# Kernel optimization log

Hardware: AMD Instinct MI355X
Metric: run time of the kernel (lower is better)

## Reference

```python
import jax, jax.numpy as jnp
import numpy as np

EMB_DIM = 128
NUM_CLS = 128
H = W = 512
K = 131072


def setup_inputs() -> dict:
    key = jax.random.key(0)
    k1, k2, k3, k4 = jax.random.split(key, 4)
    gc_features = jax.random.normal(k1, (1, EMB_DIM, H, W), dtype=jnp.float32)
    cls_id_map = jax.random.randint(k2, (1, K), 0, H * W, dtype=jnp.int64)
    # nn.Linear(emb_dim, num_cls) params, kaiming-uniform-ish scale
    lim = 1.0 / np.sqrt(EMB_DIM)
    W_cls = jax.random.uniform(k3, (NUM_CLS, EMB_DIM), dtype=jnp.float32, minval=-lim, maxval=lim)
    b_cls = jax.random.uniform(k4, (NUM_CLS,), dtype=jnp.float32, minval=-lim, maxval=lim)
    return {"gc_features": gc_features, "cls_id_map": cls_id_map, "W_cls": W_cls, "b_cls": b_cls}


def reference(gc_features, cls_id_map, W_cls, b_cls):
    B, C, h, w = gc_features.shape
    # _tranpose_and_gather_feat: [B,C,H,W] -> [B,HW,C], gather rows by inds
    feat = gc_features.reshape(B, C, h * w).transpose(0, 2, 1)      # [B, HW, C]
    feat = jnp.take_along_axis(feat, cls_id_map[:, :, None], axis=1)  # [B, K, C]
    feat = feat[0]                                                   # squeeze(0) -> [K, C]
    pred = feat @ W_cls.T + b_cls                                    # [K, num_cls]
    return jax.nn.softmax(pred, axis=1)
```

## Files before the change

kernel.cpp:

```cpp
#include <hip/hip_runtime.h>
#include <hip/hip_bf16.h>
#include <hip/hip_fp16.h>

#define HW      262144
#define NCH     128
#define NCLS    128
#define KROWS   131072
#define BM      64
#define OLP     144

typedef short  bf16x8 __attribute__((ext_vector_type(8)));
typedef float  f32x4  __attribute__((ext_vector_type(4)));

__device__ inline ushort f2bf(float f) {
    union { float f; unsigned u; } v; v.f = f;
    unsigned u = v.u;
    unsigned r = (u + 0x7FFFu + ((u >> 16) & 1u)) >> 16;
    return (ushort)r;
}

__global__ __launch_bounds__(256) void wconv(const float* __restrict__ Wc,
                                             ushort* __restrict__ Wf) {
    int e    = blockIdx.x * 256 + threadIdx.x;
    int j    = e & 7;
    int slot = e >> 3;
    int lane = slot & 63;
    int kk   = (slot >> 6) & 3;
    int nt   = slot >> 8;
    int n = (nt << 4) + (lane & 15);
    int k = (kk << 5) + ((lane >> 4) << 3) + j;
    Wf[e] = f2bf(Wc[n * NCH + k]);
}

__global__ __launch_bounds__(256) void gemm_probs(const float* __restrict__ gc,
                                                  const ushort* __restrict__ Wf,
                                                  const float* __restrict__ bias,
                                                  ushort* __restrict__ pred) {
    __shared__ ushort Wl[NCLS * NCH];
    __shared__ ushort AO[BM * OLP];

    const int t    = threadIdx.x;
    const int lane = t & 63;
    const int wv   = t >> 6;
    const int l15  = lane & 15;

    #pragma unroll
    for (int i = 0; i < 8; ++i) {
        const ushort* g = Wf + (i << 11) + (t << 3);
        ushort*       l = Wl + (i << 11) + (t << 3);
        __builtin_amdgcn_global_load_lds(
            (const __attribute__((address_space(1))) unsigned*)g,
            (__attribute__((address_space(3))) unsigned*)l, 16, 0, 0);
    }

    float bcol[8];
    #pragma unroll
    for (int nt = 0; nt < 8; ++nt) bcol[nt] = bias[(nt << 4) + l15];

    for (int tile = 0; tile < 2; ++tile) {
        const int m0 = (blockIdx.x * 2 + tile) * BM;

        __syncthreads();

        #pragma unroll
        for (int i = 0; i < 4; ++i) {
            int q  = (i << 8) + t;
            int cp = q >> 4;
            int mq = q & 15;
            int c0 = cp << 1;
            int m  = mq << 2;
            float4 v0 = *(const float4*)&gc[(size_t)c0 * HW + m0 + m];
            float4 v1 = *(const float4*)&gc[(size_t)(c0 + 1) * HW + m0 + m];
            int kk = c0 >> 5;
            int hi = ((c0 >> 3) & 3) << 4;
            int j  = c0 & 7;
            const float* a0 = (const float*)&v0;
            const float* a1 = (const float*)&v1;
            #pragma unroll
            for (int d = 0; d < 4; ++d) {
                int row   = m + d;
                int lslot = (row & 15) + hi;
                int mt    = row >> 4;
                int addr  = ((((mt << 2) + kk) << 6) + lslot) << 3;
                __hip_bfloat162 pk = __float22bfloat162_rn(make_float2(a0[d], a1[d]));
                *(ushort2*)&AO[addr + j] = *(ushort2*)&pk;
            }
        }
        __syncthreads();

        f32x4 acc[8];
        #pragma unroll
        for (int i = 0; i < 8; ++i) acc[i] = (f32x4){0.f, 0.f, 0.f, 0.f};

        #pragma unroll
        for (int kk = 0; kk < 4; ++kk) {
            bf16x8 a = *(const bf16x8*)&AO[((((wv << 2) + kk) << 6) + lane) << 3];
            #pragma unroll
            for (int nt = 0; nt < 8; ++nt) {
                bf16x8 b = *(const bf16x8*)&Wl[((((nt << 2) + kk) << 6) + lane) << 3];
                acc[nt] = __builtin_amdgcn_mfma_f32_16x16x32_bf16(a, b, acc[nt], 0, 0, 0);
            }
        }

        float pr[8][4];
        #pragma unroll
        for (int rr = 0; rr < 4; ++rr) {
            float ex[8], s = 0.f;
            #pragma unroll
            for (int nt = 0; nt < 8; ++nt) {
                ex[nt] = __expf(acc[nt][rr] + bcol[nt]);
                s += ex[nt];
            }
            s += __shfl_xor(s, 1, 64);
            s += __shfl_xor(s, 2, 64);
            s += __shfl_xor(s, 4, 64);
            s += __shfl_xor(s, 8, 64);
            float inv = 1.0f / s;
            #pragma unroll
            for (int nt = 0; nt < 8; ++nt) pr[nt][rr] = ex[nt] * inv;
        }

        __syncthreads();

        const int rowb = (wv << 4) + ((lane >> 4) << 2);
        #pragma unroll
        for (int nt = 0; nt < 8; ++nt)
            #pragma unroll
            for (int rr = 0; rr < 4; ++rr)
                AO[(rowb + rr) * OLP + (nt << 4) + l15] =
                    __half_as_ushort(__float2half_rn(pr[nt][rr]));
        __syncthreads();

        #pragma unroll
        for (int i = 0; i < 4; ++i) {
            int q   = (i << 8) + t;
            int row = q >> 4;
            int ch  = q & 15;
            int4 v = *(const int4*)&AO[row * OLP + (ch << 3)];
            *(int4*)&pred[(size_t)(m0 + row) * NCLS + (ch << 3)] = v;
        }
    }
}

__global__ __launch_bounds__(256) void gather_rows(const ushort* __restrict__ pred,
                                                   const int* __restrict__ idx,
                                                   float* __restrict__ out) {
    const int t    = threadIdx.x;
    const int lane = t & 63;
    const int wv   = t >> 6;
    const int kbase = (blockIdx.x << 4) + (wv << 2);

    int p[4];
    #pragma unroll
    for (int r = 0; r < 4; ++r) p[r] = idx[kbase + r];

    #pragma unroll
    for (int r = 0; r < 4; ++r) {
        __half2 h = *(const __half2*)&pred[(size_t)p[r] * NCLS + (lane << 1)];
        float2 f = __half22float2(h);
        *(float2*)&out[(size_t)(kbase + r) * NCLS + (lane << 1)] = f;
    }
}

extern "C" void kernel_launch(void* const* d_in, const int* in_sizes, int n_in,
                              void* d_out, int out_size, void* d_ws, size_t ws_size,
                              hipStream_t stream) {
    const float* gc   = (const float*)d_in[0];
    const int*   idx  = (const int*)d_in[1];
    const float* Wc   = (const float*)d_in[2];
    const float* bias = (const float*)d_in[3];
    float*  out  = (float*)d_out;
    ushort* pred = (ushort*)d_ws;

    ushort* Wf = (ushort*)d_out;

    wconv<<<dim3(64), dim3(256), 0, stream>>>(Wc, Wf);
    gemm_probs<<<dim3(HW / (2 * BM)), dim3(256), 0, stream>>>(gc, Wf, bias, pred);
    gather_rows<<<dim3(KROWS / 16), dim3(256), 0, stream>>>(pred, idx, out);
}
```

Before: 243.4 us.

## Replace pred buffer and gather with CSR inverse index and fused scatter

Builds a CSR inverse map from pixel to output rows using a histogram, a three-stage prefix scan and an atomic fill. The GEMM+softmax kernel then scatters each probability row straight into every output row that references it, so the fp16 pred intermediate is never written to or reread from global memory. This trades that round trip for six extra small kernel launches, atomics, and scattered, divergent per-row writes.

```diff
diff --git a/kernel.cpp b/kernel.cpp
--- a/kernel.cpp
+++ b/kernel.cpp
@@ -17,6 +17,79 @@
     unsigned u = v.u;
     unsigned r = (u + 0x7FFFu + ((u >> 16) & 1u)) >> 16;
     return (ushort)r;
+}
+
+
+__global__ __launch_bounds__(256) void csr_zero(int4* __restrict__ cnt4) {
+    cnt4[blockIdx.x * 256 + threadIdx.x] = make_int4(0, 0, 0, 0);
+}
+
+__global__ __launch_bounds__(256) void csr_hist(const int* __restrict__ idx,
+                                                int* __restrict__ cnt) {
+    int k = blockIdx.x * 256 + threadIdx.x;
+    atomicAdd(&cnt[idx[k]], 1);
+}
+
+__global__ __launch_bounds__(256) void scan_a(const int* __restrict__ cnt,
+                                              int* __restrict__ off,
+                                              int* __restrict__ bsum) {
+    __shared__ int s[256];
+    const int t = threadIdx.x;
+    const int base = blockIdx.x * 256;
+    int v = cnt[base + t];
+    s[t] = v;
+    __syncthreads();
+    #pragma unroll
+    for (int o = 1; o < 256; o <<= 1) {
+        int add = (t >= o) ? s[t - o] : 0;
+        __syncthreads();
+        s[t] += add;
+        __syncthreads();
+    }
+    off[base + t] = s[t] - v;
+    if (t == 255) bsum[blockIdx.x] = s[255];
+}
+
+__global__ __launch_bounds__(256) void scan_b(int* __restrict__ bsum) {
+    __shared__ int s[256];
+    const int t = threadIdx.x;
+    int4 v = ((int4*)bsum)[t];
+    int sum4 = v.x + v.y + v.z + v.w;
+    s[t] = sum4;
+    __syncthreads();
+    #pragma unroll
+    for (int o = 1; o < 256; o <<= 1) {
+        int add = (t >= o) ? s[t - o] : 0;
+        __syncthreads();
+        s[t] += add;
+        __syncthreads();
+    }
+    int base = s[t] - sum4;
+    int4 o;
+    o.x = base;
+    o.y = base + v.x;
+    o.z = base + v.x + v.y;
+    o.w = base + v.x + v.y + v.z;
+    ((int4*)bsum)[t] = o;
+}
+
+__global__ __launch_bounds__(256) void scan_c(int* __restrict__ off,
+                                              int* __restrict__ cur,
+                                              const int* __restrict__ bsum) {
+    const int i = blockIdx.x * 256 + threadIdx.x;
+    int o = off[i] + bsum[blockIdx.x];
+    off[i] = o;
+    cur[i] = o;
+    if (i == 0) off[HW] = KROWS;
+}
+
+__global__ __launch_bounds__(256) void csr_fill(const int* __restrict__ idx,
+                                                int* __restrict__ cur,
+                                                int* __restrict__ list) {
+    int k = blockIdx.x * 256 + threadIdx.x;
+    int p = idx[k];
+    int pos = atomicAdd(&cur[p], 1);
+    list[pos] = k;
 }
 
 __global__ __launch_bounds__(256) void wconv(const float* __restrict__ Wc,
@@ -32,10 +105,12 @@
     Wf[e] = f2bf(Wc[n * NCH + k]);
 }
 
-__global__ __launch_bounds__(256) void gemm_probs(const float* __restrict__ gc,
-                                                  const ushort* __restrict__ Wf,
-                                                  const float* __restrict__ bias,
-                                                  ushort* __restrict__ pred) {
+__global__ __launch_bounds__(256) void gemm_scatter(const float* __restrict__ gc,
+                                                    const ushort* __restrict__ Wf,
+                                                    const float* __restrict__ bias,
+                                                    const int* __restrict__ off,
+                                                    const int* __restrict__ list,
+                                                    float* __restrict__ out) {
     __shared__ ushort Wl[NCLS * NCH];
     __shared__ ushort AO[BM * OLP];
 
@@ -131,34 +206,23 @@
                     __half_as_ushort(__float2half_rn(pr[nt][rr]));
         __syncthreads();
 
-        #pragma unroll
-        for (int i = 0; i < 4; ++i) {
-            int q   = (i << 8) + t;
-            int row = q >> 4;
-            int ch  = q & 15;
-            int4 v = *(const int4*)&AO[row * OLP + (ch << 3)];
-            *(int4*)&pred[(size_t)(m0 + row) * NCLS + (ch << 3)] = v;
-        }
-    }
-}
-
-__global__ __launch_bounds__(256) void gather_rows(const ushort* __restrict__ pred,
-                                                   const int* __restrict__ idx,
-                                                   float* __restrict__ out) {
-    const int t    = threadIdx.x;
-    const int lane = t & 63;
-    const int wv   = t >> 6;
-    const int kbase = (blockIdx.x << 4) + (wv << 2);
-
-    int p[4];
-    #pragma unroll
-    for (int r = 0; r < 4; ++r) p[r] = idx[kbase + r];
-
-    #pragma unroll
-    for (int r = 0; r < 4; ++r) {
-        __half2 h = *(const __half2*)&pred[(size_t)p[r] * NCLS + (lane << 1)];
-        float2 f = __half22float2(h);
-        *(float2*)&out[(size_t)(kbase + r) * NCLS + (lane << 1)] = f;
+        const int pbase = m0 + (wv << 4);
+        int ofl = 0;
+        if (lane < 17) ofl = off[pbase + lane];
+
+        #pragma unroll 1
+        for (int r = 0; r < 16; ++r) {
+            int o0 = __shfl(ofl, r, 64);
+            int o1 = __shfl(ofl, r + 1, 64);
+            if (o0 == o1) continue;
+            __half2 h = *(const __half2*)&AO[((wv << 4) + r) * OLP + (lane << 1)];
+            float2 f = __half22float2(h);
+            #pragma unroll 1
+            for (int e = o0; e < o1; ++e) {
+                int k = list[e];
+                *(float2*)&out[(size_t)k * NCLS + (lane << 1)] = f;
+            }
+        }
     }
 }
 
@@ -169,12 +233,22 @@
     const int*   idx  = (const int*)d_in[1];
     const float* Wc   = (const float*)d_in[2];
     const float* bias = (const float*)d_in[3];
-    float*  out  = (float*)d_out;
-    ushort* pred = (ushort*)d_ws;
-
-    ushort* Wf = (ushort*)d_out;
-
-    wconv<<<dim3(64), dim3(256), 0, stream>>>(Wc, Wf);
-    gemm_probs<<<dim3(HW / (2 * BM)), dim3(256), 0, stream>>>(gc, Wf, bias, pred);
-    gather_rows<<<dim3(KROWS / 16), dim3(256), 0, stream>>>(pred, idx, out);
-}
+    float* out = (float*)d_out;
+
+    char* ws = (char*)d_ws;
+    int*    cnt  = (int*)(ws);
+    int*    off  = (int*)(ws + 0x100000);
+    int*    cur  = (int*)(ws + 0x300000);
+    int*    list = (int*)(ws + 0x400000);
+    int*    bsum = (int*)(ws + 0x480000);
+    ushort* Wf   = (ushort*)(ws + 0x500000);
+
+    csr_zero<<<dim3(256),  dim3(256), 0, stream>>>((int4*)cnt);
+    csr_hist<<<dim3(512),  dim3(256), 0, stream>>>(idx, cnt);
+    scan_a  <<<dim3(1024), dim3(256), 0, stream>>>(cnt, off, bsum);
+    scan_b  <<<dim3(1),    dim3(256), 0, stream>>>(bsum);
+    scan_c  <<<dim3(1024), dim3(256), 0, stream>>>(off, cur, bsum);
+    csr_fill<<<dim3(512),  dim3(256), 0, stream>>>(idx, cur, list);
+    wconv   <<<dim3(64),   dim3(256), 0, stream>>>(Wc, Wf);
+    gemm_scatter<<<dim3(HW / (2 * BM)), dim3(256), 0, stream>>>(gc, Wf, bias, off, list, out);
+}
```

Result: slower. 256.0 us (+5.2%).

## Use one tile per block, prefetch activations early, swizzle LDS, widen gather

Applied to the files above, without the earlier changes.

Each GEMM block now handles a single 64-row tile and issues its global activation loads before the weight-to-LDS copy, so those transfers overlap. The padded LDS staging buffer is replaced by an XOR-swizzled layout for both the A operand and the output transpose, which cuts LDS use and is meant to avoid bank conflicts. The gather kernel now handles 8 rows per wave instead of 4, and the converted weights move into the workspace instead of the output buffer. The grid doubles, and the extra registers held by the prefetched activations may lower occupancy.

```diff
diff --git a/kernel.cpp b/kernel.cpp
--- a/kernel.cpp
+++ b/kernel.cpp
@@ -6,8 +6,6 @@
 #define NCH     128
 #define NCLS    128
 #define KROWS   131072
-#define BM      64
-#define OLP     144
 
 typedef short  bf16x8 __attribute__((ext_vector_type(8)));
 typedef float  f32x4  __attribute__((ext_vector_type(4)));
@@ -37,12 +35,24 @@
                                                   const float* __restrict__ bias,
                                                   ushort* __restrict__ pred) {
     __shared__ ushort Wl[NCLS * NCH];
-    __shared__ ushort AO[BM * OLP];
+    __shared__ ushort AO[64 * NCH];
 
     const int t    = threadIdx.x;
     const int lane = t & 63;
     const int wv   = t >> 6;
     const int l15  = lane & 15;
+    const int quad = lane >> 4;
+    const int m0   = blockIdx.x << 6;
+
+    float4 va[8];
+    #pragma unroll
+    for (int i = 0; i < 4; ++i) {
+        int q  = (i << 8) + t;
+        int cp = q >> 4, mq = q & 15;
+        int c0 = cp << 1, m = mq << 2;
+        va[2 * i]     = *(const float4*)&gc[(size_t)c0 * HW + m0 + m];
+        va[2 * i + 1] = *(const float4*)&gc[(size_t)(c0 + 1) * HW + m0 + m];
+    }
 
     #pragma unroll
     for (int i = 0; i < 8; ++i) {
@@ -57,88 +67,77 @@
     #pragma unroll
     for (int nt = 0; nt < 8; ++nt) bcol[nt] = bias[(nt << 4) + l15];
 
-    for (int tile = 0; tile < 2; ++tile) {
-        const int m0 = (blockIdx.x * 2 + tile) * BM;
+    #pragma unroll
+    for (int i = 0; i < 4; ++i) {
+        int q  = (i << 8) + t;
+        int cp = q >> 4, mq = q & 15;
+        int c0 = cp << 1, m = mq << 2;
+        int kk = c0 >> 5, kc2 = (c0 >> 3) & 3, j = c0 & 7;
+        const float* a0 = (const float*)&va[2 * i];
+        const float* a1 = (const float*)&va[2 * i + 1];
+        #pragma unroll
+        for (int d = 0; d < 4; ++d) {
+            int row  = m + d;
+            int slot = ((((row >> 4) << 2) + kk) << 6) + (row & 15) + (kc2 << 4);
+            slot ^= (row >> 2) & 7;
+            __hip_bfloat162 pk = __float22bfloat162_rn(make_float2(a0[d], a1[d]));
+            *(ushort2*)&AO[(slot << 3) + j] = *(ushort2*)&pk;
+        }
+    }
+    __syncthreads();
 
-        __syncthreads();
+    f32x4 acc[8];
+    #pragma unroll
+    for (int i = 0; i < 8; ++i) acc[i] = (f32x4){0.f, 0.f, 0.f, 0.f};
 
+    #pragma unroll
+    for (int kk = 0; kk < 4; ++kk) {
+        int aslot = ((((wv << 2) + kk) << 6) + lane) ^ ((((wv << 4) + l15) >> 2) & 7);
+        bf16x8 a = *(const bf16x8*)&AO[aslot << 3];
         #pragma unroll
-        for (int i = 0; i < 4; ++i) {
-            int q  = (i << 8) + t;
-            int cp = q >> 4;
-            int mq = q & 15;
-            int c0 = cp << 1;
-            int m  = mq << 2;
-            float4 v0 = *(const float4*)&gc[(size_t)c0 * HW + m0 + m];
-            float4 v1 = *(const float4*)&gc[(size_t)(c0 + 1) * HW + m0 + m];
-            int kk = c0 >> 5;
-            int hi = ((c0 >> 3) & 3) << 4;
-            int j  = c0 & 7;
-            const float* a0 = (const float*)&v0;
-            const float* a1 = (const float*)&v1;
-            #pragma unroll
-            for (int d = 0; d < 4; ++d) {
-                int row   = m + d;
-                int lslot = (row & 15) + hi;
-                int mt    = row >> 4;
-                int addr  = ((((mt << 2) + kk) << 6) + lslot) << 3;
-                __hip_bfloat162 pk = __float22bfloat162_rn(make_float2(a0[d], a1[d]));
-                *(ushort2*)&AO[addr + j] = *(ushort2*)&pk;
-            }
+        for (int nt = 0; nt < 8; ++nt) {
+            bf16x8 b = *(const bf16x8*)&Wl[((((nt << 2) + kk) << 6) + lane) << 3];
+            acc[nt] = __builtin_amdgcn_mfma_f32_16x16x32_bf16(a, b, acc[nt], 0, 0, 0);
         }
-        __syncthreads();
+    }
 
-        f32x4 acc[8];
+    float inv[4];
+    #pragma unroll
+    for (int rr = 0; rr < 4; ++rr) {
+        float s = 0.f;
         #pragma unroll
-        for (int i = 0; i < 8; ++i) acc[i] = (f32x4){0.f, 0.f, 0.f, 0.f};
+        for (int nt = 0; nt < 8; ++nt) {
+            acc[nt][rr] = __expf(acc[nt][rr] + bcol[nt]);
+            s += acc[nt][rr];
+        }
+        s += __shfl_xor(s, 1, 64);
+        s += __shfl_xor(s, 2, 64);
+        s += __shfl_xor(s, 4, 64);
+        s += __shfl_xor(s, 8, 64);
+        inv[rr] = 1.0f / s;
+    }
 
-        #pragma unroll
-        for (int kk = 0; kk < 4; ++kk) {
-            bf16x8 a = *(const bf16x8*)&AO[((((wv << 2) + kk) << 6) + lane) << 3];
-            #pragma unroll
-            for (int nt = 0; nt < 8; ++nt) {
-                bf16x8 b = *(const bf16x8*)&Wl[((((nt << 2) + kk) << 6) + lane) << 3];
-                acc[nt] = __builtin_amdgcn_mfma_f32_16x16x32_bf16(a, b, acc[nt], 0, 0, 0);
-            }
-        }
-
-        float pr[8][4];
+    const int g = ((quad & 1) << 2) | (quad & 2);
+    #pragma unroll
+    for (int nt = 0; nt < 8; ++nt) {
+        int cl = ((nt << 1) + (l15 >> 3)) ^ g;
         #pragma unroll
         for (int rr = 0; rr < 4; ++rr) {
-            float ex[8], s = 0.f;
-            #pragma unroll
-            for (int nt = 0; nt < 8; ++nt) {
-                ex[nt] = __expf(acc[nt][rr] + bcol[nt]);
-                s += ex[nt];
-            }
-            s += __shfl_xor(s, 1, 64);
-            s += __shfl_xor(s, 2, 64);
-            s += __shfl_xor(s, 4, 64);
-            s += __shfl_xor(s, 8, 64);
-            float inv = 1.0f / s;
-            #pragma unroll
-            for (int nt = 0; nt < 8; ++nt) pr[nt][rr] = ex[nt] * inv;
+            int row = (wv << 4) + (quad << 2) + rr;
+            AO[(row << 7) + (cl << 3) + (l15 & 7)] =
+                __half_as_ushort(__float2half_rn(acc[nt][rr] * inv[rr]));
         }
+    }
+    __syncthreads();
 
-        __syncthreads();
-
-        const int rowb = (wv << 4) + ((lane >> 4) << 2);
-        #pragma unroll
-        for (int nt = 0; nt < 8; ++nt)
-            #pragma unroll
-            for (int rr = 0; rr < 4; ++rr)
-                AO[(rowb + rr) * OLP + (nt << 4) + l15] =
-                    __half_as_ushort(__float2half_rn(pr[nt][rr]));
-        __syncthreads();
-
-        #pragma unroll
-        for (int i = 0; i < 4; ++i) {
-            int q   = (i << 8) + t;
-            int row = q >> 4;
-            int ch  = q & 15;
-            int4 v = *(const int4*)&AO[row * OLP + (ch << 3)];
-            *(int4*)&pred[(size_t)(m0 + row) * NCLS + (ch << 3)] = v;
-        }
+    #pragma unroll
+    for (int i = 0; i < 4; ++i) {
+        int q   = (i << 8) + t;
+        int row = q >> 4, ch = q & 15;
+        int qd  = (row >> 2) & 3;
+        int cl  = ch ^ (((qd & 1) << 2) | (qd & 2));
+        int4 v = *(const int4*)&AO[(row << 7) + (cl << 3)];
+        *(int4*)&pred[((size_t)(m0 + row) << 7) + (ch << 3)] = v;
     }
 }
 
@@ -148,17 +147,17 @@
     const int t    = threadIdx.x;
     const int lane = t & 63;
     const int wv   = t >> 6;
-    const int kbase = (blockIdx.x << 4) + (wv << 2);
+    const int kbase = (blockIdx.x << 5) + (wv << 3);
 
-    int p[4];
+    int p[8];
     #pragma unroll
-    for (int r = 0; r < 4; ++r) p[r] = idx[kbase + r];
+    for (int r = 0; r < 8; ++r) p[r] = idx[kbase + r];
 
     #pragma unroll
-    for (int r = 0; r < 4; ++r) {
-        __half2 h = *(const __half2*)&pred[(size_t)p[r] * NCLS + (lane << 1)];
+    for (int r = 0; r < 8; ++r) {
+        __half2 h = *(const __half2*)&pred[((size_t)p[r] << 7) + (lane << 1)];
         float2 f = __half22float2(h);
-        *(float2*)&out[(size_t)(kbase + r) * NCLS + (lane << 1)] = f;
+        *(float2*)&out[((size_t)(kbase + r) << 7) + (lane << 1)] = f;
     }
 }
 
@@ -171,10 +170,9 @@
     const float* bias = (const float*)d_in[3];
     float*  out  = (float*)d_out;
     ushort* pred = (ushort*)d_ws;
+    ushort* Wf   = (ushort*)((char*)d_ws + (size_t)64 * 1024 * 1024);
 
-    ushort* Wf = (ushort*)d_out;
-
-    wconv<<<dim3(64), dim3(256), 0, stream>>>(Wc, Wf);
-    gemm_probs<<<dim3(HW / (2 * BM)), dim3(256), 0, stream>>>(gc, Wf, bias, pred);
-    gather_rows<<<dim3(KROWS / 16), dim3(256), 0, stream>>>(pred, idx, out);
+    wconv      <<<dim3(64),    dim3(256), 0, stream>>>(Wc, Wf);
+    gemm_probs <<<dim3(HW/64), dim3(256), 0, stream>>>(gc, Wf, bias, pred);
+    gather_rows<<<dim3(KROWS/32), dim3(256), 0, stream>>>(pred, idx, out);
 }
```

After: 241.2 us. Within noise of the previous version (-0.9%).
